# Performance work log

Measured on AMD Instinct MI355X. Metric: run time of the kernel, lower is better.

Reference implementation:

```python
import jax, jax.numpy as jnp
import numpy as np

B, C, H, W = 2, 256, 64, 64
KEEP = 0.1


def setup_inputs() -> dict:
    key = jax.random.key(0)
    ks = jax.random.split(key, 7)
    s = 0.05  # small init for 1x1-conv weights
    return {
        "x": jax.random.normal(ks[0], (B, C, H, W), dtype=jnp.float32),
        "Wq": jax.random.normal(ks[1], (C, C), dtype=jnp.float32) * s,
        "bq": jax.random.normal(ks[2], (C,), dtype=jnp.float32) * s,
        "Wk": jax.random.normal(ks[3], (C, C), dtype=jnp.float32) * s,
        "bk": jax.random.normal(ks[4], (C,), dtype=jnp.float32) * s,
        "Wv": jax.random.normal(ks[5], (C, C), dtype=jnp.float32) * s,
        "bv": jax.random.normal(ks[6], (C,), dtype=jnp.float32) * s,
    }


def reference(x, Wq, bq, Wk, bk, Wv, bv):
    b, c, h, w = x.shape
    n = h * w

    def proj(Wm, bm):
        # 1x1 conv == per-pixel linear; output as [B, N, C] tokens
        return jnp.einsum('bchw,oc->bhwo', x, Wm).reshape(b, n, c) + bm

    q = proj(Wq, bq)
    k = proj(Wk, bk)
    v = proj(Wv, bv)

    scores = jnp.einsum('bnc,bmc->bnm', q, k) / (c ** 0.5)  # [B, N, N]
    k_keep = max(1, int(KEEP * n))

    vals, idx = jax.lax.top_k(scores, k_keep)  # [B, N, k_keep]
    # softmax over -inf-masked scores == softmax over topk vals scattered into zeros
    probs = jax.nn.softmax(vals, axis=-1)
    attn = jnp.zeros_like(scores).at[
        jnp.arange(b)[:, None, None], jnp.arange(n)[None, :, None], idx
    ].set(probs)

    out = jnp.einsum('bnm,bmc->bnc', attn, v)  # [B, N, C]
    return out.transpose(0, 2, 1).reshape(b, c, h, w)
```

## Files before the change

### kernel.cpp

```cpp
#include <hip/hip_runtime.h>
#include <hip/hip_bf16.h>
#include <math.h>

#define BATCH 2
#define CC    256
#define NN    4096
#define KK    409
#define KCAT  768
#define SCALE 0.0625f
#define PSTRIDE 8192

typedef _Float16 half8 __attribute__((ext_vector_type(8)));
typedef float    floatx4 __attribute__((ext_vector_type(4)));

typedef __attribute__((address_space(3))) unsigned       lds_u32;
typedef __attribute__((address_space(1))) const unsigned glb_u32;
__device__ __forceinline__ void gload16(const void* g, void* l) {
    __builtin_amdgcn_global_load_lds((glb_u32*)g, (lds_u32*)l, 16, 0, 0);
}

__device__ __forceinline__ unsigned fkey(float f) {
    unsigned u = __float_as_uint(f);
    return (u & 0x80000000u) ? ~u : (u | 0x80000000u);
}
__device__ __forceinline__ float keyToF(unsigned k) {
    unsigned u = (k & 0x80000000u) ? (k ^ 0x80000000u) : ~k;
    return __uint_as_float(u);
}

__global__ __launch_bounds__(256) void xpose_kernel(
        const float* __restrict__ x, _Float16* __restrict__ xcat) {
    __shared__ float xs[64][68];
    const int t  = threadIdx.x;
    const int n0 = blockIdx.x * 64;
    const int c0 = blockIdx.y * 64;
    const int b  = blockIdx.z;

    {
        const int ci = t >> 2;
        const int j  = (t & 3) * 16;
        const float* xp = x + ((size_t)((b << 8) + c0 + ci)) * NN + n0 + j;
        float4 a0 = ((const float4*)xp)[0];
        float4 a1 = ((const float4*)xp)[1];
        float4 a2 = ((const float4*)xp)[2];
        float4 a3 = ((const float4*)xp)[3];
        *(float4*)&xs[ci][j]      = a0;
        *(float4*)&xs[ci][j + 4]  = a1;
        *(float4*)&xs[ci][j + 8]  = a2;
        *(float4*)&xs[ci][j + 12] = a3;
    }
    __syncthreads();

    const int n = t >> 2;
    const int g0 = t & 3;
    _Float16* xr = xcat + ((size_t)(b * NN + n0 + n)) * KCAT + c0;
#pragma unroll
    for (int gg = 0; gg < 2; gg++) {
        int g = g0 + gg * 4;
        half8 hi, lo;
#pragma unroll
        for (int k = 0; k < 8; k++) {
            float v = xs[g * 8 + k][n];
            _Float16 h = (_Float16)v;
            hi[k] = h;
            lo[k] = (_Float16)(v - (float)h);
        }
        *(half8*)(xr + g * 8)       = hi;
        *(half8*)(xr + 256 + g * 8) = lo;
        *(half8*)(xr + 512 + g * 8) = hi;
    }
}

__global__ void wcat_kernel(const float* __restrict__ Wq,
                            const float* __restrict__ Wk,
                            const float* __restrict__ Wv,
                            _Float16* __restrict__ Wcat) {
    int mat = blockIdx.x >> 8;
    int o   = blockIdx.x & 255;
    int c   = threadIdx.x;
    const float* W = (mat == 0) ? Wq : (mat == 1) ? Wk : Wv;
    float v = W[o * 256 + c];
    _Float16 hi = (_Float16)v;
    _Float16 lo = (_Float16)(v - (float)hi);
    _Float16* wr = Wcat + ((size_t)(mat * 256 + o)) * KCAT;
    wr[c] = hi; wr[256 + c] = hi; wr[512 + c] = lo;
}

__global__ __launch_bounds__(256) void proj_gemm(
        const _Float16* __restrict__ xcat, const _Float16* __restrict__ Wcat,
        const float* __restrict__ bq, const float* __restrict__ bk,
        const float* __restrict__ bv,
        _Float16* __restrict__ Qcat, _Float16* __restrict__ Kcat,
        _Float16* __restrict__ Vt) {
    __shared__ _Float16 As[128][72];
    __shared__ _Float16 Bs[128][72];

    const int t    = threadIdx.x;
    const int wave = t >> 6;
    const int l    = t & 63;
    const int wr   = wave >> 1;
    const int wc   = wave & 1;
    const int mat  = blockIdx.z;

    int bym, bxn;
    if (mat < 2) { bym = blockIdx.x >> 1; bxn = blockIdx.x & 1; }
    else         { bym = blockIdx.x & 1;  bxn = blockIdx.x >> 1; }

    const int r = t >> 1;
    const int h = t & 1;

    const _Float16* Abase;
    const _Float16* Bbase;
    if (mat < 2) {
        Abase = xcat + ((size_t)(bym * 128 + r)) * KCAT + h * 32;
        Bbase = Wcat + ((size_t)(mat * 256 + bxn * 128 + r)) * KCAT + h * 32;
    } else {
        Abase = Wcat + ((size_t)(512 + bym * 128 + r)) * KCAT + h * 32;
        Bbase = xcat + ((size_t)(bxn * 128 + r)) * KCAT + h * 32;
    }

    floatx4 acc[4][4];
#pragma unroll
    for (int i = 0; i < 4; i++)
#pragma unroll
        for (int j = 0; j < 4; j++) acc[i][j] = (floatx4)0.0f;

    const int rowA = l & 15;
    const int koff = (l >> 4) * 8;

    for (int kc = 0; kc < KCAT; kc += 64) {
        const uint4* ap = (const uint4*)(Abase + kc);
        const uint4* bp = (const uint4*)(Bbase + kc);
        uint4 a0 = ap[0], a1 = ap[1], a2 = ap[2], a3 = ap[3];
        uint4 b0 = bp[0], b1 = bp[1], b2 = bp[2], b3 = bp[3];
        *(uint4*)&As[r][h * 32]      = a0;
        *(uint4*)&As[r][h * 32 + 8]  = a1;
        *(uint4*)&As[r][h * 32 + 16] = a2;
        *(uint4*)&As[r][h * 32 + 24] = a3;
        *(uint4*)&Bs[r][h * 32]      = b0;
        *(uint4*)&Bs[r][h * 32 + 8]  = b1;
        *(uint4*)&Bs[r][h * 32 + 16] = b2;
        *(uint4*)&Bs[r][h * 32 + 24] = b3;
        __syncthreads();
#pragma unroll
        for (int ks = 0; ks < 64; ks += 32) {
            half8 af[4], bf[4];
#pragma unroll
            for (int mi = 0; mi < 4; mi++)
                af[mi] = *(const half8*)&As[wr * 64 + mi * 16 + rowA][ks + koff];
#pragma unroll
            for (int ni = 0; ni < 4; ni++)
                bf[ni] = *(const half8*)&Bs[wc * 64 + ni * 16 + rowA][ks + koff];
#pragma unroll
            for (int mi = 0; mi < 4; mi++)
#pragma unroll
                for (int ni = 0; ni < 4; ni++)
                    acc[mi][ni] = __builtin_amdgcn_mfma_f32_16x16x32_f16(
                        af[mi], bf[ni], acc[mi][ni], 0, 0, 0);
        }
        __syncthreads();
    }

    if (mat < 2) {
        const float* bias = (mat == 0) ? bq : bk;
        _Float16* Out = (mat == 0) ? Qcat : Kcat;
#pragma unroll
        for (int ni = 0; ni < 4; ni++) {
            int ch = bxn * 128 + wc * 64 + ni * 16 + (l & 15);
            float bb = bias[ch];
#pragma unroll
            for (int mi = 0; mi < 4; mi++)
#pragma unroll
                for (int rg = 0; rg < 4; rg++) {
                    int token = bym * 128 + wr * 64 + mi * 16 + (l >> 4) * 4 + rg;
                    float v = acc[mi][ni][rg] + bb;
                    _Float16 hi = (_Float16)v;
                    _Float16 lo = (_Float16)(v - (float)hi);
                    _Float16* p = Out + (size_t)token * KCAT + ch;
                    if (mat == 0) { p[0] = hi; p[256] = lo; p[512] = hi; }
                    else          { p[0] = hi; p[256] = hi; p[512] = lo; }
                }
        }
    } else {
#pragma unroll
        for (int mi = 0; mi < 4; mi++)
#pragma unroll
            for (int rg = 0; rg < 4; rg++) {
                int ch = bym * 128 + wr * 64 + mi * 16 + (l >> 4) * 4 + rg;
                float bb = bv[ch];
#pragma unroll
                for (int ni = 0; ni < 4; ni++) {
                    int col = bxn * 128 + wc * 64 + ni * 16 + (l & 15);
                    int b = col >> 12, n = col & 4095;
                    Vt[((size_t)((b << 8) + ch)) * NN + n] =
                        (_Float16)(acc[mi][ni][rg] + bb);
                }
            }
    }
}

__global__ __launch_bounds__(512, 2) void score_gemm(
        const _Float16* __restrict__ Qcat, const _Float16* __restrict__ Kcat,
        float* __restrict__ S) {
    __shared__ _Float16 As[256][64];
    __shared__ _Float16 Bs[256][64];

    const int t    = threadIdx.x;
    const int wave = t >> 6;
    const int l    = t & 63;
    const int wr   = wave >> 1;
    const int wc   = wave & 1;
    const int bxn  = blockIdx.x;
    const int bym  = blockIdx.y;
    const int b    = blockIdx.z;

    const int lr = l >> 3;
    const int gg = (l & 7) ^ lr;

    const _Float16* At = Qcat + ((size_t)((b << 12) + bym * 256)) * KCAT;
    const _Float16* Bt = Kcat + ((size_t)((b << 12) + bxn * 256)) * KCAT;
    const size_t lane_off = (size_t)lr * KCAT + gg * 8;

    floatx4 acc[4][8];
#pragma unroll
    for (int i = 0; i < 4; i++)
#pragma unroll
        for (int j = 0; j < 8; j++) acc[i][j] = (floatx4)0.0f;

    const int rowA = l & 15;
    const int sg0  = (l >> 4) ^ (l & 7);
    const int sg1  = sg0 ^ 4;

    for (int kc = 0; kc < KCAT; kc += 64) {
#pragma unroll
        for (int s = 0; s < 4; s++) {
            const int seg = wave * 4 + s;
            gload16(At + (size_t)seg * 8 * KCAT + lane_off + kc, &As[seg * 8][0]);
            gload16(Bt + (size_t)seg * 8 * KCAT + lane_off + kc, &Bs[seg * 8][0]);
        }
        __syncthreads();
#pragma unroll
        for (int ks = 0; ks < 2; ks++) {
            const int sg = ks ? sg1 : sg0;
            half8 af[4], bf[8];
#pragma unroll
            for (int mi = 0; mi < 4; mi++)
                af[mi] = *(const half8*)&As[wr * 64 + mi * 16 + rowA][sg * 8];
#pragma unroll
            for (int ni = 0; ni < 8; ni++)
                bf[ni] = *(const half8*)&Bs[wc * 128 + ni * 16 + rowA][sg * 8];
#pragma unroll
            for (int mi = 0; mi < 4; mi++)
#pragma unroll
                for (int ni = 0; ni < 8; ni++)
                    acc[mi][ni] = __builtin_amdgcn_mfma_f32_16x16x32_f16(
                        af[mi], bf[ni], acc[mi][ni], 0, 0, 0);
        }
        __syncthreads();
    }

    float* Sb = S + ((size_t)b << 24);
#pragma unroll
    for (int mi = 0; mi < 4; mi++)
#pragma unroll
        for (int ni = 0; ni < 8; ni++) {
            int col = bxn * 256 + wc * 128 + ni * 16 + (l & 15);
#pragma unroll
            for (int rg = 0; rg < 4; rg++) {
                int row = bym * 256 + wr * 64 + mi * 16 + (l >> 4) * 4 + rg;
                Sb[((size_t)row << 12) + col] = acc[mi][ni][rg] * SCALE;
            }
        }
}

__global__ __launch_bounds__(256) void select_scatter(
        const float* __restrict__ S, _Float16* __restrict__ P) {
    __shared__ unsigned hist[256];
    __shared__ unsigned scan[256];
    __shared__ unsigned candKey[NN];
    __shared__ unsigned wred[4];
    __shared__ float    fmn[4], fmx[4], wsum[4];
    __shared__ unsigned sh_d, sh_cntgt;
    __shared__ int      sh_ncand;

    const int t = threadIdx.x;
    const int l = t & 63;
    const int w = t >> 6;

    float    val[16];
    unsigned ukey[16];
    {
        const float*  Srow = S + ((size_t)blockIdx.x << 12);
        const float4* sp   = (const float4*)(Srow + t * 16);
#pragma unroll
        for (int jj = 0; jj < 4; jj++) {
            float4 v = sp[jj];
            val[jj * 4 + 0] = v.x; val[jj * 4 + 1] = v.y;
            val[jj * 4 + 2] = v.z; val[jj * 4 + 3] = v.w;
        }
#pragma unroll
        for (int j = 0; j < 16; j++) ukey[j] = fkey(val[j]);
    }

    float lmin = val[0], lmax = val[0];
#pragma unroll
    for (int j = 1; j < 16; j++) {
        lmin = fminf(lmin, val[j]); lmax = fmaxf(lmax, val[j]);
    }
#pragma unroll
    for (int off = 32; off > 0; off >>= 1) {
        float a = __shfl_down(lmin, off);
        float b = __shfl_down(lmax, off);
        if (l + off < 64) { lmin = fminf(lmin, a); lmax = fmaxf(lmax, b); }
    }
    if (l == 0) { fmn[w] = lmin; fmx[w] = lmax; }

    hist[t] = 0u;
    if (t == 0) sh_ncand = 0;
    __syncthreads();
    const float fmin = fminf(fminf(fmn[0], fmn[1]), fminf(fmn[2], fmn[3]));
    const float fmax = fmaxf(fmaxf(fmx[0], fmx[1]), fmaxf(fmx[2], fmx[3]));
    const float range = fmax - fmin;
    const float bscale = (range > 1e-20f) ? 255.0f / range : 0.0f;

    auto binOf = [&](float v) -> int {
        int bin = (int)((v - fmin) * bscale);
        return bin < 0 ? 0 : (bin > 255 ? 255 : bin);
    };

#pragma unroll
    for (int j = 0; j < 16; j++) atomicAdd(&hist[binOf(val[j])], 1u);
    __syncthreads();

    int rem = KK;

    auto find_digit = [&](int remv) {
        unsigned v = hist[t];
#pragma unroll
        for (int off = 1; off < 64; off <<= 1) {
            unsigned o = __shfl_down(v, off);
            if (l + off < 64) v += o;
        }
        if (l == 0) wred[w] = v;
        __syncthreads();
        unsigned add = 0u;
#pragma unroll
        for (int w2 = 0; w2 < 4; w2++) if (w2 > w) add += wred[w2];
        scan[t] = v + add;
        __syncthreads();
        unsigned sufd  = scan[t];
        unsigned sufd1 = (t < 255) ? scan[t + 1] : 0u;
        if (sufd >= (unsigned)remv && sufd1 < (unsigned)remv) {
            sh_d = (unsigned)t; sh_cntgt = sufd1;
        }
        __syncthreads();
    };

    find_digit(rem);
    const int dbin = (int)sh_d;
    rem -= (int)sh_cntgt;

#pragma unroll
    for (int j = 0; j < 16; j++) {
        if (binOf(val[j]) == dbin) {
            int slot = atomicAdd(&sh_ncand, 1);
            candKey[slot] = ukey[j];
        }
    }
    __syncthreads();
    const int nc = sh_ncand;

    unsigned prefix = 0u;
    for (int pass = 0; pass < 4; pass++) {
        const int shift = 24 - 8 * pass;
        hist[t] = 0u;
        __syncthreads();
        for (int i = t; i < nc; i += 256) {
            unsigned u2 = candKey[i];
            if (pass == 0 || (u2 >> (shift + 8)) == (prefix >> (shift + 8)))
                atomicAdd(&hist[(u2 >> shift) & 255u], 1u);
        }
        __syncthreads();
        find_digit(rem);
        prefix |= (sh_d << shift);
        rem -= (int)sh_cntgt;
    }
    const unsigned T = prefix;
    const int need = rem;
    const float mT = keyToF(T);

    int eqc = 0;
#pragma unroll
    for (int j = 0; j < 16; j++) if (ukey[j] == T) eqc++;
    int vinc = eqc;
#pragma unroll
    for (int off = 1; off < 64; off <<= 1) {
        int o = __shfl_up(vinc, off);
        if (l >= off) vinc += o;
    }
    if (l == 63) wred[w] = (unsigned)vinc;
    __syncthreads();
    int addlow = 0;
#pragma unroll
    for (int w2 = 0; w2 < 4; w2++) if (w2 < w) addlow += (int)wred[w2];
    const int eqexcl = vinc - eqc + addlow;

    float pv[16];
    float le = 0.f;
#pragma unroll
    for (int j = 0; j < 16; j++) {
        float e = 0.f;
        if (ukey[j] > T) { e = __expf(val[j] - mT); le += e; }
        pv[j] = e;
    }
    if (eqc) {
        int seen = 0;
#pragma unroll
        for (int j = 0; j < 16; j++) {
            if (ukey[j] == T) {
                if (eqexcl + seen < need) { pv[j] = 1.0f; le += 1.0f; }
                seen++;
            }
        }
    }

#pragma unroll
    for (int off = 32; off > 0; off >>= 1) {
        float o = __shfl_down(le, off);
        if (l + off < 64) le += o;
    }
    if (l == 0) wsum[w] = le;
    __syncthreads();
    const float inv = 1.0f / (wsum[0] + wsum[1] + wsum[2] + wsum[3]);

    half8 ra, rb;
#pragma unroll
    for (int j = 0; j < 8; j++) {
        ra[j] = (_Float16)(pv[j] * inv);
        rb[j] = (_Float16)(pv[j + 8] * inv);
    }
    _Float16* Pr = P + (size_t)blockIdx.x * PSTRIDE + t * 16;
    *(half8*)Pr       = ra;
    *(half8*)(Pr + 8) = rb;
}

__global__ __launch_bounds__(256) void av_gemm(
        const _Float16* __restrict__ Vt, const _Float16* __restrict__ P,
        float* __restrict__ out) {
    __shared__ _Float16 As[64][72];
    __shared__ _Float16 Bs[64][72];

    const int t    = threadIdx.x;
    const int wave = t >> 6;
    const int l    = t & 63;
    const int wr   = wave >> 1;
    const int wc   = wave & 1;
    const int bxn  = blockIdx.x;
    const int byc  = blockIdx.y;
    const int b    = blockIdx.z;

    const int r = t >> 2;
    const int q = t & 3;

    const _Float16* Abase = Vt + ((size_t)((b << 8) + byc * 64 + r)) * NN + q * 16;
    const _Float16* Bbase = P + ((size_t)(b * NN + bxn * 64 + r)) * PSTRIDE + q * 16;

    floatx4 acc[2][2];
#pragma unroll
    for (int i = 0; i < 2; i++)
#pragma unroll
        for (int j = 0; j < 2; j++) acc[i][j] = (floatx4)0.0f;

    const int rowA = l & 15;
    const int koff = (l >> 4) * 8;

    for (int kc = 0; kc < NN; kc += 64) {
        const uint4* ap = (const uint4*)(Abase + kc);
        const uint4* bp = (const uint4*)(Bbase + kc);
        uint4 a0 = ap[0], a1 = ap[1];
        uint4 b0 = bp[0], b1 = bp[1];
        *(uint4*)&As[r][q * 16]     = a0;
        *(uint4*)&As[r][q * 16 + 8] = a1;
        *(uint4*)&Bs[r][q * 16]     = b0;
        *(uint4*)&Bs[r][q * 16 + 8] = b1;
        __syncthreads();
#pragma unroll
        for (int ks = 0; ks < 64; ks += 32) {
            half8 af[2], bf[2];
#pragma unroll
            for (int mi = 0; mi < 2; mi++)
                af[mi] = *(const half8*)&As[wr * 32 + mi * 16 + rowA][ks + koff];
#pragma unroll
            for (int ni = 0; ni < 2; ni++)
                bf[ni] = *(const half8*)&Bs[wc * 32 + ni * 16 + rowA][ks + koff];
#pragma unroll
            for (int mi = 0; mi < 2; mi++)
#pragma unroll
                for (int ni = 0; ni < 2; ni++)
                    acc[mi][ni] = __builtin_amdgcn_mfma_f32_16x16x32_f16(
                        af[mi], bf[ni], acc[mi][ni], 0, 0, 0);
        }
        __syncthreads();
    }

#pragma unroll
    for (int mi = 0; mi < 2; mi++)
#pragma unroll
        for (int ni = 0; ni < 2; ni++) {
            int col = bxn * 64 + wc * 32 + ni * 16 + (l & 15);
#pragma unroll
            for (int rg = 0; rg < 4; rg++) {
                int row = byc * 64 + wr * 32 + mi * 16 + (l >> 4) * 4 + rg;
                out[((size_t)((b << 8) + row) << 12) + col] = acc[mi][ni][rg];
            }
        }
}

extern "C" void kernel_launch(void* const* d_in, const int* in_sizes, int n_in,
                              void* d_out, int out_size, void* d_ws, size_t ws_size,
                              hipStream_t stream) {
    const float* x  = (const float*)d_in[0];
    const float* Wq = (const float*)d_in[1];
    const float* bq = (const float*)d_in[2];
    const float* Wk = (const float*)d_in[3];
    const float* bk = (const float*)d_in[4];
    const float* Wv = (const float*)d_in[5];
    const float* bv = (const float*)d_in[6];
    float* out = (float*)d_out;

    char* ws = (char*)d_ws;
    _Float16* Wcat = (_Float16*)ws;
    _Float16* Qcat = (_Float16*)(ws + 1179648);
    _Float16* Kcat = (_Float16*)(ws + 1179648 + 12582912);
    _Float16* Vt   = (_Float16*)(ws + 1179648 + 2 * 12582912);
    float*    S    = (float*)   (ws + 1179648 + 2 * 12582912 + 4194304);
    _Float16* xcat = (_Float16*)S;
    _Float16* P    = (_Float16*)S;

    xpose_kernel<<<dim3(64, 4, BATCH), 256, 0, stream>>>(x, xcat);
    wcat_kernel<<<768, 256, 0, stream>>>(Wq, Wk, Wv, Wcat);
    proj_gemm<<<dim3(128, 1, 3), 256, 0, stream>>>(xcat, Wcat, bq, bk, bv,
                                                   Qcat, Kcat, Vt);
    score_gemm<<<dim3(16, 16, BATCH), 512, 0, stream>>>(Qcat, Kcat, S);
    select_scatter<<<BATCH * NN, 256, 0, stream>>>(S, P);
    av_gemm<<<dim3(64, 4, BATCH), 256, 0, stream>>>(Vt, P, out);
}
```

Baseline: 263.9 us.

## Use direct global-to-LDS loads with XOR swizzle, fuse prep kernels, add wave-level select

Merges the weight-conversion kernel into the transpose kernel as an extra grid slice, which saves a launch. proj_gemm and av_gemm now stage tiles with global_load_lds 16-byte loads into unpadded, XOR-swizzled LDS. av_gemm also loads 128-wide K chunks into two buffers per barrier, halving the number of syncs. select_scatter adds a single-wave shuffle rank path when there are 64 or fewer candidates, skipping the four-pass radix histogram. The swizzle indexing has to match between the load and read sides, and the direct LDS loads remove the register staging.

New measurement: 243.6 us. 1.08x faster.

```diff
diff --git a/kernel.cpp b/kernel.cpp
--- a/kernel.cpp
+++ b/kernel.cpp
@@ -28,10 +28,31 @@
     return __uint_as_float(u);
 }
 
-__global__ __launch_bounds__(256) void xpose_kernel(
-        const float* __restrict__ x, _Float16* __restrict__ xcat) {
+__global__ __launch_bounds__(256) void xpose_wcat_kernel(
+        const float* __restrict__ x,
+        const float* __restrict__ Wq, const float* __restrict__ Wk,
+        const float* __restrict__ Wv,
+        _Float16* __restrict__ xcat, _Float16* __restrict__ Wcat) {
+    const int t  = threadIdx.x;
+    if (blockIdx.y == 4) {
+        int idx = (blockIdx.z * 64 + blockIdx.x) * 256 + t;
+#pragma unroll
+        for (int k = 0; k < 6; k++) {
+            int e = idx + k * 32768;
+            int mat = e >> 16;
+            int o   = (e >> 8) & 255;
+            int c   = e & 255;
+            const float* W = (mat == 0) ? Wq : (mat == 1) ? Wk : Wv;
+            float v = W[o * 256 + c];
+            _Float16 hi = (_Float16)v;
+            _Float16 lo = (_Float16)(v - (float)hi);
+            _Float16* wr = Wcat + ((size_t)(mat * 256 + o)) * KCAT;
+            wr[c] = hi; wr[256 + c] = hi; wr[512 + c] = lo;
+        }
+        return;
+    }
+
     __shared__ float xs[64][68];
-    const int t  = threadIdx.x;
     const int n0 = blockIdx.x * 64;
     const int c0 = blockIdx.y * 64;
     const int b  = blockIdx.z;
@@ -71,29 +92,14 @@
     }
 }
 
-__global__ void wcat_kernel(const float* __restrict__ Wq,
-                            const float* __restrict__ Wk,
-                            const float* __restrict__ Wv,
-                            _Float16* __restrict__ Wcat) {
-    int mat = blockIdx.x >> 8;
-    int o   = blockIdx.x & 255;
-    int c   = threadIdx.x;
-    const float* W = (mat == 0) ? Wq : (mat == 1) ? Wk : Wv;
-    float v = W[o * 256 + c];
-    _Float16 hi = (_Float16)v;
-    _Float16 lo = (_Float16)(v - (float)hi);
-    _Float16* wr = Wcat + ((size_t)(mat * 256 + o)) * KCAT;
-    wr[c] = hi; wr[256 + c] = hi; wr[512 + c] = lo;
-}
-
 __global__ __launch_bounds__(256) void proj_gemm(
         const _Float16* __restrict__ xcat, const _Float16* __restrict__ Wcat,
         const float* __restrict__ bq, const float* __restrict__ bk,
         const float* __restrict__ bv,
         _Float16* __restrict__ Qcat, _Float16* __restrict__ Kcat,
         _Float16* __restrict__ Vt) {
-    __shared__ _Float16 As[128][72];
-    __shared__ _Float16 Bs[128][72];
+    __shared__ _Float16 As[128][64];
+    __shared__ _Float16 Bs[128][64];
 
     const int t    = threadIdx.x;
     const int wave = t >> 6;
@@ -106,18 +112,19 @@
     if (mat < 2) { bym = blockIdx.x >> 1; bxn = blockIdx.x & 1; }
     else         { bym = blockIdx.x & 1;  bxn = blockIdx.x >> 1; }
 
-    const int r = t >> 1;
-    const int h = t & 1;
-
-    const _Float16* Abase;
-    const _Float16* Bbase;
+    const int lr = l >> 3;
+    const int gg = (l & 7) ^ lr;
+
+    const _Float16* At;
+    const _Float16* Bt;
     if (mat < 2) {
-        Abase = xcat + ((size_t)(bym * 128 + r)) * KCAT + h * 32;
-        Bbase = Wcat + ((size_t)(mat * 256 + bxn * 128 + r)) * KCAT + h * 32;
+        At = xcat + ((size_t)(bym * 128)) * KCAT;
+        Bt = Wcat + ((size_t)(mat * 256 + bxn * 128)) * KCAT;
     } else {
-        Abase = Wcat + ((size_t)(512 + bym * 128 + r)) * KCAT + h * 32;
-        Bbase = xcat + ((size_t)(bxn * 128 + r)) * KCAT + h * 32;
-    }
+        At = Wcat + ((size_t)(512 + bym * 128)) * KCAT;
+        Bt = xcat + ((size_t)(bxn * 128)) * KCAT;
+    }
+    const size_t lane_off = (size_t)lr * KCAT + gg * 8;
 
     floatx4 acc[4][4];
 #pragma unroll
@@ -126,31 +133,27 @@
         for (int j = 0; j < 4; j++) acc[i][j] = (floatx4)0.0f;
 
     const int rowA = l & 15;
-    const int koff = (l >> 4) * 8;
+    const int sg0  = (l >> 4) ^ (l & 7);
+    const int sg1  = sg0 ^ 4;
 
     for (int kc = 0; kc < KCAT; kc += 64) {
-        const uint4* ap = (const uint4*)(Abase + kc);
-        const uint4* bp = (const uint4*)(Bbase + kc);
-        uint4 a0 = ap[0], a1 = ap[1], a2 = ap[2], a3 = ap[3];
-        uint4 b0 = bp[0], b1 = bp[1], b2 = bp[2], b3 = bp[3];
-        *(uint4*)&As[r][h * 32]      = a0;
-        *(uint4*)&As[r][h * 32 + 8]  = a1;
-        *(uint4*)&As[r][h * 32 + 16] = a2;
-        *(uint4*)&As[r][h * 32 + 24] = a3;
-        *(uint4*)&Bs[r][h * 32]      = b0;
-        *(uint4*)&Bs[r][h * 32 + 8]  = b1;
-        *(uint4*)&Bs[r][h * 32 + 16] = b2;
-        *(uint4*)&Bs[r][h * 32 + 24] = b3;
-        __syncthreads();
-#pragma unroll
-        for (int ks = 0; ks < 64; ks += 32) {
+#pragma unroll
+        for (int s = 0; s < 4; s++) {
+            const int seg = wave * 4 + s;
+            gload16(At + (size_t)seg * 8 * KCAT + lane_off + kc, &As[seg * 8][0]);
+            gload16(Bt + (size_t)seg * 8 * KCAT + lane_off + kc, &Bs[seg * 8][0]);
+        }
+        __syncthreads();
+#pragma unroll
+        for (int ks = 0; ks < 2; ks++) {
+            const int sg = ks ? sg1 : sg0;
             half8 af[4], bf[4];
 #pragma unroll
             for (int mi = 0; mi < 4; mi++)
-                af[mi] = *(const half8*)&As[wr * 64 + mi * 16 + rowA][ks + koff];
+                af[mi] = *(const half8*)&As[wr * 64 + mi * 16 + rowA][sg * 8];
 #pragma unroll
             for (int ni = 0; ni < 4; ni++)
-                bf[ni] = *(const half8*)&Bs[wc * 64 + ni * 16 + rowA][ks + koff];
+                bf[ni] = *(const half8*)&Bs[wc * 64 + ni * 16 + rowA][sg * 8];
 #pragma unroll
             for (int mi = 0; mi < 4; mi++)
 #pragma unroll
@@ -280,8 +283,8 @@
     __shared__ unsigned candKey[NN];
     __shared__ unsigned wred[4];
     __shared__ float    fmn[4], fmx[4], wsum[4];
-    __shared__ unsigned sh_d, sh_cntgt;
-    __shared__ int      sh_ncand;
+    __shared__ unsigned sh_d, sh_cntgt, sh_T;
+    __shared__ int      sh_ncand, sh_need;
 
     const int t = threadIdx.x;
     const int l = t & 63;
@@ -370,23 +373,40 @@
     __syncthreads();
     const int nc = sh_ncand;
 
-    unsigned prefix = 0u;
-    for (int pass = 0; pass < 4; pass++) {
-        const int shift = 24 - 8 * pass;
-        hist[t] = 0u;
-        __syncthreads();
-        for (int i = t; i < nc; i += 256) {
-            unsigned u2 = candKey[i];
-            if (pass == 0 || (u2 >> (shift + 8)) == (prefix >> (shift + 8)))
-                atomicAdd(&hist[(u2 >> shift) & 255u], 1u);
-        }
-        __syncthreads();
-        find_digit(rem);
-        prefix |= (sh_d << shift);
-        rem -= (int)sh_cntgt;
-    }
-    const unsigned T = prefix;
-    const int need = rem;
+    if (nc <= 64) {
+        if (w == 0) {
+            unsigned kl = (l < nc) ? candKey[l] : 0u;
+            int r = 0, g = 0;
+            for (int j = 0; j < 64; j++) {
+                unsigned kj = __shfl(kl, j);
+                bool gt = kj > kl;
+                g += gt ? 1 : 0;
+                r += (gt || (kj == kl && j < l)) ? 1 : 0;
+            }
+            if (r == rem - 1) { sh_T = kl; sh_need = rem - g; }
+        }
+    } else {
+        unsigned prefix = 0u;
+        int rem2 = rem;
+        for (int pass = 0; pass < 4; pass++) {
+            const int shift = 24 - 8 * pass;
+            hist[t] = 0u;
+            __syncthreads();
+            for (int i = t; i < nc; i += 256) {
+                unsigned u2 = candKey[i];
+                if (pass == 0 || (u2 >> (shift + 8)) == (prefix >> (shift + 8)))
+                    atomicAdd(&hist[(u2 >> shift) & 255u], 1u);
+            }
+            __syncthreads();
+            find_digit(rem2);
+            prefix |= (sh_d << shift);
+            rem2 -= (int)sh_cntgt;
+        }
+        if (t == 0) { sh_T = prefix; sh_need = rem2; }
+    }
+    __syncthreads();
+    const unsigned T = sh_T;
+    const int need = sh_need;
     const float mT = keyToF(T);
 
     int eqc = 0;
@@ -447,8 +467,8 @@
 __global__ __launch_bounds__(256) void av_gemm(
         const _Float16* __restrict__ Vt, const _Float16* __restrict__ P,
         float* __restrict__ out) {
-    __shared__ _Float16 As[64][72];
-    __shared__ _Float16 Bs[64][72];
+    __shared__ _Float16 As0[64][64], As1[64][64];
+    __shared__ _Float16 Bs0[64][64], Bs1[64][64];
 
     const int t    = threadIdx.x;
     const int wave = t >> 6;
@@ -459,11 +479,13 @@
     const int byc  = blockIdx.y;
     const int b    = blockIdx.z;
 
-    const int r = t >> 2;
-    const int q = t & 3;
-
-    const _Float16* Abase = Vt + ((size_t)((b << 8) + byc * 64 + r)) * NN + q * 16;
-    const _Float16* Bbase = P + ((size_t)(b * NN + bxn * 64 + r)) * PSTRIDE + q * 16;
+    const int lr = l >> 3;
+    const int gg = (l & 7) ^ lr;
+
+    const _Float16* At = Vt + ((size_t)((b << 8) + byc * 64)) * NN;
+    const _Float16* Bt = P + ((size_t)(b * NN + bxn * 64)) * PSTRIDE;
+    const size_t lane_offA = (size_t)lr * NN + gg * 8;
+    const size_t lane_offB = (size_t)lr * PSTRIDE + gg * 8;
 
     floatx4 acc[2][2];
 #pragma unroll
@@ -471,28 +493,31 @@
 #pragma unroll
         for (int j = 0; j < 2; j++) acc[i][j] = (floatx4)0.0f;
 
-    const int rowA = l & 15;
-    const int koff = (l >> 4) * 8;
-
-    for (int kc = 0; kc < NN; kc += 64) {
-        const uint4* ap = (const uint4*)(Abase + kc);
-        const uint4* bp = (const uint4*)(Bbase + kc);
-        uint4 a0 = ap[0], a1 = ap[1];
-        uint4 b0 = bp[0], b1 = bp[1];
-        *(uint4*)&As[r][q * 16]     = a0;
-        *(uint4*)&As[r][q * 16 + 8] = a1;
-        *(uint4*)&Bs[r][q * 16]     = b0;
-        *(uint4*)&Bs[r][q * 16 + 8] = b1;
-        __syncthreads();
-#pragma unroll
-        for (int ks = 0; ks < 64; ks += 32) {
+    const int rowA   = l & 15;
+    const int sgbase = (l >> 4) ^ (l & 7);
+
+    for (int kc = 0; kc < NN; kc += 128) {
+#pragma unroll
+        for (int s = 0; s < 2; s++) {
+            const int seg = wave * 2 + s;
+            gload16(At + (size_t)seg * 8 * NN + lane_offA + kc,           &As0[seg * 8][0]);
+            gload16(At + (size_t)seg * 8 * NN + lane_offA + kc + 64,      &As1[seg * 8][0]);
+            gload16(Bt + (size_t)seg * 8 * PSTRIDE + lane_offB + kc,      &Bs0[seg * 8][0]);
+            gload16(Bt + (size_t)seg * 8 * PSTRIDE + lane_offB + kc + 64, &Bs1[seg * 8][0]);
+        }
+        __syncthreads();
+#pragma unroll
+        for (int st = 0; st < 4; st++) {
+            const _Float16 (*Ap)[64] = (st < 2) ? As0 : As1;
+            const _Float16 (*Bp)[64] = (st < 2) ? Bs0 : Bs1;
+            const int sg = sgbase ^ ((st & 1) ? 4 : 0);
             half8 af[2], bf[2];
 #pragma unroll
             for (int mi = 0; mi < 2; mi++)
-                af[mi] = *(const half8*)&As[wr * 32 + mi * 16 + rowA][ks + koff];
+                af[mi] = *(const half8*)&Ap[wr * 32 + mi * 16 + rowA][sg * 8];
 #pragma unroll
             for (int ni = 0; ni < 2; ni++)
-                bf[ni] = *(const half8*)&Bs[wc * 32 + ni * 16 + rowA][ks + koff];
+                bf[ni] = *(const half8*)&Bp[wc * 32 + ni * 16 + rowA][sg * 8];
 #pragma unroll
             for (int mi = 0; mi < 2; mi++)
 #pragma unroll
@@ -537,8 +562,8 @@
     _Float16* xcat = (_Float16*)S;
     _Float16* P    = (_Float16*)S;
 
-    xpose_kernel<<<dim3(64, 4, BATCH), 256, 0, stream>>>(x, xcat);
-    wcat_kernel<<<768, 256, 0, stream>>>(Wq, Wk, Wv, Wcat);
+    xpose_wcat_kernel<<<dim3(64, 5, BATCH), 256, 0, stream>>>(x, Wq, Wk, Wv,
+                                                              xcat, Wcat);
     proj_gemm<<<dim3(128, 1, 3), 256, 0, stream>>>(xcat, Wcat, bq, bk, bv,
                                                    Qcat, Kcat, Vt);
     score_gemm<<<dim3(16, 16, BATCH), 512, 0, stream>>>(Qcat, Kcat, S);
```
